# Performance work log

Measured on AMD Instinct MI355X. Metric: run time of the kernel, lower is better.

## Reference

```python
import jax, jax.numpy as jnp
import numpy as np

N_NODES = 50000
N_EDGES = 800000
IN_CH = 256
H1, D1 = 4, 64   # layer 1: 4 heads x 64 -> 256
H2, D2 = 1, 64   # output layer: 1 head x 64
NEG_SLOPE = 0.2  # DGL GATConv default


def _leaky_relu(x):
    return jnp.where(x >= 0, x, NEG_SLOPE * x)


def gat_conv(h, src, dst, W, attn_l, attn_r, bias, res_W, num_heads, out_feats, apply_elu):
    """DGL GATConv (eval mode, feat_drop=attn_drop=0).
    h: (N, F_in); src/dst: (E,) edge endpoints (edge u->v aggregates at v).
    W: (F_in, H*D); attn_l/attn_r: (H, D); bias: (H*D,); res_W: (F_in, H*D) or None.
    Returns (N, H, D).
    """
    N = h.shape[0]
    ft = (h @ W).reshape(N, num_heads, out_feats)            # (N,H,D)
    el = jnp.sum(ft * attn_l, axis=-1)                        # (N,H)
    er = jnp.sum(ft * attn_r, axis=-1)                        # (N,H)
    e = _leaky_relu(el[src] + er[dst])                        # (E,H)
    # segment softmax over incoming edges of each dst node
    emax = jax.ops.segment_max(e, dst, num_segments=N)        # (N,H)
    emax = jax.lax.stop_gradient(emax)
    ee = jnp.exp(e - emax[dst])                               # (E,H)
    denom = jax.ops.segment_sum(ee, dst, num_segments=N)      # (N,H)
    a = ee / denom[dst]                                       # (E,H)
    msg = ft[src] * a[:, :, None]                             # (E,H,D)
    rst = jax.ops.segment_sum(msg, dst, num_segments=N)       # (N,H,D)
    if res_W is not None:
        rst = rst + (h @ res_W).reshape(N, num_heads, out_feats)
    rst = rst + bias.reshape(num_heads, out_feats)
    if apply_elu:
        rst = jax.nn.elu(rst)
    return rst


def setup_inputs() -> dict:
    key = jax.random.key(0)
    ks = jax.random.split(key, 12)
    feat = jax.random.normal(ks[0], (N_NODES, IN_CH), dtype=jnp.float32)
    src = jax.random.randint(ks[1], (N_EDGES,), 0, N_NODES)
    dst = jax.random.randint(ks[2], (N_EDGES,), 0, N_NODES)
    s = 0.1
    W1 = jax.random.normal(ks[3], (IN_CH, H1 * D1), dtype=jnp.float32) * s
    al1 = jax.random.normal(ks[4], (H1, D1), dtype=jnp.float32) * s
    ar1 = jax.random.normal(ks[5], (H1, D1), dtype=jnp.float32) * s
    b1 = jnp.zeros((H1 * D1,), dtype=jnp.float32)
    W2 = jax.random.normal(ks[6], (H1 * D1, H2 * D2), dtype=jnp.float32) * s
    al2 = jax.random.normal(ks[7], (H2, D2), dtype=jnp.float32) * s
    ar2 = jax.random.normal(ks[8], (H2, D2), dtype=jnp.float32) * s
    b2 = jnp.zeros((H2 * D2,), dtype=jnp.float32)
    resW2 = jax.random.normal(ks[9], (H1 * D1, H2 * D2), dtype=jnp.float32) * s
    return {"feat": feat, "src": src, "dst": dst,
            "W1": W1, "al1": al1, "ar1": ar1, "b1": b1,
            "W2": W2, "al2": al2, "ar2": ar2, "b2": b2, "resW2": resW2}


def reference(feat, src, dst, W1, al1, ar1, b1, W2, al2, ar2, b2, resW2):
    # Layer 1: 4 heads, ELU, no residual (first DGL layer built without residual)
    h = gat_conv(feat, src, dst, W1, al1, ar1, b1, None, H1, D1, True)
    h = h.reshape(N_NODES, H1 * D1)  # flatten(1)
    # Layer 2: 1 head, residual (linear res_fc since 256 != 64), no activation
    h = gat_conv(h, src, dst, W2, al2, ar2, b2, resW2, H2, D2, False)
    return h.mean(axis=1)  # mean over output heads -> (N, out_channels)
```

## Files before the change

### kernel.cpp

```cpp
#include <hip/hip_runtime.h>
#include <math.h>

#define N_NODES 50000
#define N_EDGES 800000
#define ELL_W 64
#define CNT_STRIDE 16

#define E_SPLIT 400000
#define CONV_BLKS 1792
#define SCAT_BLKS 512

typedef __attribute__((ext_vector_type(8))) short bf16x8;
typedef __attribute__((ext_vector_type(4))) float f32x4;

__device__ __forceinline__ float leaky(float x) { return x >= 0.f ? x : 0.2f * x; }
__device__ __forceinline__ unsigned short f2bf(float f) {
  unsigned u = __float_as_uint(f);
  return (unsigned short)((u + 0x7fffu + ((u >> 16) & 1u)) >> 16);
}
__device__ __forceinline__ float bflo(unsigned u) { return __uint_as_float(u << 16); }
__device__ __forceinline__ float bfhi(unsigned u) { return __uint_as_float(u & 0xffff0000u); }
__device__ __forceinline__ unsigned pack2(float a, float b) {
  return (unsigned)f2bf(a) | ((unsigned)f2bf(b) << 16);
}

__device__ __forceinline__ void scat4(const int* __restrict__ src, const int* __restrict__ dst,
                                      int* __restrict__ cnt, unsigned short* __restrict__ ell,
                                      int e) {
  int4 d4 = *(const int4*)(dst + e);
  int4 s4 = *(const int4*)(src + e);
  int sl;
  sl = atomicAdd(cnt + d4.x * CNT_STRIDE, 1);
  if (sl < ELL_W) __builtin_nontemporal_store((unsigned short)s4.x, ell + d4.x * ELL_W + sl);
  sl = atomicAdd(cnt + d4.y * CNT_STRIDE, 1);
  if (sl < ELL_W) __builtin_nontemporal_store((unsigned short)s4.y, ell + d4.y * ELL_W + sl);
  sl = atomicAdd(cnt + d4.z * CNT_STRIDE, 1);
  if (sl < ELL_W) __builtin_nontemporal_store((unsigned short)s4.z, ell + d4.z * ELL_W + sl);
  sl = atomicAdd(cnt + d4.w * CNT_STRIDE, 1);
  if (sl < ELL_W) __builtin_nontemporal_store((unsigned short)s4.w, ell + d4.w * ELL_W + sl);
}

__launch_bounds__(256)
__global__ void prep_k(const float* __restrict__ feat, const float* __restrict__ W1,
                       const float* __restrict__ W2, const float* __restrict__ resW2,
                       short* __restrict__ featb, short* __restrict__ Wt1,
                       short* __restrict__ Wt2, const int* __restrict__ src,
                       const int* __restrict__ dst, int* __restrict__ cnt,
                       unsigned short* __restrict__ ell) {
  if (blockIdx.x < SCAT_BLKS) {
    const int gtid = blockIdx.x * 256 + threadIdx.x;
    const int gsz = SCAT_BLKS * 256;
    for (int q = gtid; q < E_SPLIT / 4; q += gsz) scat4(src, dst, cnt, ell, q * 4);
    return;
  }
  const int gtid = (blockIdx.x - SCAT_BLKS) * 256 + threadIdx.x;
  const int gsz = CONV_BLKS * 256;
  for (int idx = gtid; idx < 256 * 256; idx += gsz) {
    int n = idx >> 8, k = idx & 255;
    Wt1[idx] = (short)f2bf(W1[(size_t)k * 256 + n]);
  }
  for (int idx = gtid; idx < 128 * 256; idx += gsz) {
    int n = idx >> 8, k = idx & 255;
    float v = (n < 64) ? W2[(size_t)k * 64 + n] : resW2[(size_t)k * 64 + (n - 64)];
    Wt2[idx] = (short)f2bf(v);
  }
  const float4* f4 = (const float4*)feat;
  uint2* fb2 = (uint2*)featb;
  for (int idx = gtid; idx < N_NODES * 64; idx += gsz) {
    float4 f = f4[idx];
    uint2 o;
    o.x = pack2(f.x, f.y);
    o.y = pack2(f.z, f.w);
    fb2[idx] = o;
  }
}

template <int MODE, bool SCAT>
__launch_bounds__(256)
__global__ void mfma_gemm_k(const short* __restrict__ A, const short* __restrict__ Bt,
                            const float* __restrict__ bias, const float* __restrict__ al,
                            const float* __restrict__ ar, float* __restrict__ elp,
                            float* __restrict__ erp, short* __restrict__ Cb,
                            float* __restrict__ Cf, const int* __restrict__ src,
                            const int* __restrict__ dst, int* __restrict__ cnt,
                            unsigned short* __restrict__ ell, int M, int K, int N) {
  constexpr int EPI_COLS = (MODE == 0) ? 136 : 72;
  union SharedU {
    struct { short As[4][128][8]; short Bs[4][128][8]; } ab;
    short epi[128 * EPI_COLS];
  };
  __shared__ SharedU sh;

  if (SCAT && blockIdx.y == 0) {
    const int gtid = blockIdx.x * 256 + threadIdx.x;
    const int gsz = gridDim.x * 256;
    for (int q = gtid; q < (N_EDGES - E_SPLIT) / 4; q += gsz)
      scat4(src, dst, cnt, ell, E_SPLIT + q * 4);
    return;
  }
  const int tid = threadIdx.x;
  const int bm0 = blockIdx.x * 128;
  const int bn0 = (SCAT ? ((int)blockIdx.y - 1) : (int)blockIdx.y) * 128;
  const int wave = tid >> 6, lane = tid & 63;
  const int wm = (wave & 1) * 64, wn = (wave >> 1) * 64;
  const int q = lane >> 4, r16 = lane & 15;
  const int srow = tid >> 1, sk = (tid & 1) * 16, sq = (tid & 1) * 2;
  f32x4 acc[4][4] = {};

  for (int k0 = 0; k0 < K; k0 += 32) {
    {
      uint4 v0 = {0, 0, 0, 0}, v1 = {0, 0, 0, 0};
      if (bm0 + srow < M) {
        const uint4* p = (const uint4*)(A + (size_t)(bm0 + srow) * K + k0 + sk);
        v0 = p[0];
        v1 = p[1];
      }
      *(uint4*)&sh.ab.As[sq][srow][0] = v0;
      *(uint4*)&sh.ab.As[sq + 1][srow][0] = v1;
    }
    {
      const uint4* p = (const uint4*)(Bt + (size_t)(bn0 + srow) * K + k0 + sk);
      *(uint4*)&sh.ab.Bs[sq][srow][0] = p[0];
      *(uint4*)&sh.ab.Bs[sq + 1][srow][0] = p[1];
    }
    __syncthreads();
    bf16x8 af[4], bfr[4];
#pragma unroll
    for (int i = 0; i < 4; ++i) af[i] = *(const bf16x8*)&sh.ab.As[q][wm + i * 16 + r16][0];
#pragma unroll
    for (int j = 0; j < 4; ++j) bfr[j] = *(const bf16x8*)&sh.ab.Bs[q][wn + j * 16 + r16][0];
#pragma unroll
    for (int i = 0; i < 4; ++i)
#pragma unroll
      for (int j = 0; j < 4; ++j)
        acc[i][j] = __builtin_amdgcn_mfma_f32_16x16x32_bf16(af[i], bfr[j], acc[i][j], 0, 0, 0);
    __syncthreads();
  }

  if (MODE == 0 || wn == 0) {
    const int head = (bn0 + wn) >> 6;
    float alv[4], arv[4];
#pragma unroll
    for (int j = 0; j < 4; ++j) {
      alv[j] = al[((MODE == 0) ? head * 64 : 0) + j * 16 + r16];
      arv[j] = ar[((MODE == 0) ? head * 64 : 0) + j * 16 + r16];
    }
#pragma unroll
    for (int i = 0; i < 4; ++i) {
#pragma unroll
      for (int reg = 0; reg < 4; ++reg) {
        float dl = acc[i][0][reg] * alv[0] + acc[i][1][reg] * alv[1] +
                   acc[i][2][reg] * alv[2] + acc[i][3][reg] * alv[3];
        float dr = acc[i][0][reg] * arv[0] + acc[i][1][reg] * arv[1] +
                   acc[i][2][reg] * arv[2] + acc[i][3][reg] * arv[3];
#pragma unroll
        for (int mm = 1; mm < 16; mm <<= 1) {
          dl += __shfl_xor(dl, mm);
          dr += __shfl_xor(dr, mm);
        }
        int row_g = bm0 + wm + i * 16 + q * 4 + reg;
        if (r16 == 0 && row_g < M) {
          if (MODE == 0) {
            elp[(size_t)row_g * 4 + head] = dl;
            erp[(size_t)row_g * 4 + head] = dr;
          } else {
            elp[row_g] = dl;
            erp[row_g] = dr;
          }
        }
      }
    }
  }

  if (MODE == 0) {
#pragma unroll
    for (int i = 0; i < 4; ++i)
#pragma unroll
      for (int reg = 0; reg < 4; ++reg) {
        int row = wm + i * 16 + q * 4 + reg;
#pragma unroll
        for (int j = 0; j < 4; ++j)
          sh.epi[row * EPI_COLS + wn + j * 16 + r16] = (short)f2bf(acc[i][j][reg]);
      }
    __syncthreads();
#pragma unroll
    for (int k = 0; k < 8; ++k) {
      int c = k * 256 + tid;
      int row = c >> 4, cc = c & 15;
      int row_g = bm0 + row;
      if (row_g < M) {
        uint4 v = *(const uint4*)&sh.epi[row * EPI_COLS + cc * 8];
        *(uint4*)(Cb + (size_t)row_g * N + bn0 + cc * 8) = v;
      }
    }
  } else {
    if (wn == 0) {
#pragma unroll
      for (int i = 0; i < 4; ++i)
#pragma unroll
        for (int reg = 0; reg < 4; ++reg) {
          int row = wm + i * 16 + q * 4 + reg;
#pragma unroll
          for (int j = 0; j < 4; ++j)
            sh.epi[row * EPI_COLS + j * 16 + r16] = (short)f2bf(acc[i][j][reg]);
        }
    } else {
#pragma unroll
      for (int i = 0; i < 4; ++i)
#pragma unroll
        for (int reg = 0; reg < 4; ++reg) {
          int row_g = bm0 + wm + i * 16 + q * 4 + reg;
          if (row_g >= M) continue;
#pragma unroll
          for (int j = 0; j < 4; ++j) {
            int col = j * 16 + r16;
            Cf[(size_t)row_g * 64 + col] = acc[i][j][reg] + bias[col];
          }
        }
    }
    __syncthreads();
#pragma unroll
    for (int k = 0; k < 4; ++k) {
      int c = k * 256 + tid;
      int row = c >> 3, cc = c & 7;
      int row_g = bm0 + row;
      if (row_g < M) {
        uint4 v = *(const uint4*)&sh.epi[row * EPI_COLS + cc * 8];
        *(uint4*)(Cb + (size_t)row_g * 64 + cc * 8) = v;
      }
    }
  }
}

__launch_bounds__(256)
__global__ void agg1_k(const unsigned short* __restrict__ ell, const int* __restrict__ cnt,
                       const float* __restrict__ el, const float* __restrict__ er,
                       const short* __restrict__ ft, const float* __restrict__ bias,
                       short* __restrict__ h1) {
  int node = blockIdx.x * 4 + (threadIdx.x >> 6);
  int lane = threadIdx.x & 63;
  if (node >= N_NODES) return;
  int deg = min(cnt[node * CNT_STRIDE], ELL_W);
  const unsigned short* row = ell + node * ELL_W;
  const int half = lane >> 5, l5 = lane & 31, h = l5 >> 3;
  float erh = er[(size_t)node * 4 + h];
  float denom = 0.f;
  float acc[8] = {0.f, 0.f, 0.f, 0.f, 0.f, 0.f, 0.f, 0.f};
  int i = 0;
  for (; i + 8 <= deg; i += 8) {
    int s[4];
#pragma unroll
    for (int k = 0; k < 4; ++k) s[k] = row[i + k * 2 + half];
    float e[4];
#pragma unroll
    for (int k = 0; k < 4; ++k) e[k] = leaky(el[(size_t)s[k] * 4 + h] + erh);
    uint4 u[4];
#pragma unroll
    for (int k = 0; k < 4; ++k) u[k] = *(const uint4*)(ft + (size_t)s[k] * 256 + l5 * 8);
    float w[4];
#pragma unroll
    for (int k = 0; k < 4; ++k) w[k] = __expf(e[k]);
#pragma unroll
    for (int k = 0; k < 4; ++k) {
      denom += w[k];
      acc[0] += w[k] * bflo(u[k].x);
      acc[1] += w[k] * bfhi(u[k].x);
      acc[2] += w[k] * bflo(u[k].y);
      acc[3] += w[k] * bfhi(u[k].y);
      acc[4] += w[k] * bflo(u[k].z);
      acc[5] += w[k] * bfhi(u[k].z);
      acc[6] += w[k] * bflo(u[k].w);
      acc[7] += w[k] * bfhi(u[k].w);
    }
  }
  for (; i < deg; i += 2) {
    int idx = i + half;
    bool v = idx < deg;
    int s = v ? (int)row[idx] : (int)row[i];
    float e = leaky(el[(size_t)s * 4 + h] + erh);
    uint4 u = *(const uint4*)(ft + (size_t)s * 256 + l5 * 8);
    float w = v ? __expf(e) : 0.f;
    denom += w;
    acc[0] += w * bflo(u.x);
    acc[1] += w * bfhi(u.x);
    acc[2] += w * bflo(u.y);
    acc[3] += w * bfhi(u.y);
    acc[4] += w * bflo(u.z);
    acc[5] += w * bfhi(u.z);
    acc[6] += w * bflo(u.w);
    acc[7] += w * bfhi(u.w);
  }
  denom += __shfl_xor(denom, 32);
#pragma unroll
  for (int k = 0; k < 8; ++k) acc[k] += __shfl_xor(acc[k], 32);
  if (half == 0) {
    float inv = (deg > 0) ? 1.f / denom : 0.f;
    float4 b0 = *(const float4*)(bias + l5 * 8);
    float4 b1 = *(const float4*)(bias + l5 * 8 + 4);
    float v[8];
    v[0] = acc[0] * inv + b0.x;
    v[1] = acc[1] * inv + b0.y;
    v[2] = acc[2] * inv + b0.z;
    v[3] = acc[3] * inv + b0.w;
    v[4] = acc[4] * inv + b1.x;
    v[5] = acc[5] * inv + b1.y;
    v[6] = acc[6] * inv + b1.z;
    v[7] = acc[7] * inv + b1.w;
#pragma unroll
    for (int k = 0; k < 8; ++k) v[k] = v[k] > 0.f ? v[k] : expm1f(v[k]);
    uint4 o;
    o.x = pack2(v[0], v[1]);
    o.y = pack2(v[2], v[3]);
    o.z = pack2(v[4], v[5]);
    o.w = pack2(v[6], v[7]);
    *(uint4*)(h1 + (size_t)node * 256 + l5 * 8) = o;
  }
}

__launch_bounds__(256)
__global__ void agg2_k(const unsigned short* __restrict__ ell, const int* __restrict__ cnt,
                       const float* __restrict__ el, const float* __restrict__ er,
                       const short* __restrict__ ft, float* __restrict__ out) {
  int node = blockIdx.x * 4 + (threadIdx.x >> 6);
  int lane = threadIdx.x & 63;
  if (node >= N_NODES) return;
  int deg = min(cnt[node * CNT_STRIDE], ELL_W);
  const unsigned short* row = ell + node * ELL_W;
  const int qtr = lane >> 4, l4 = lane & 15;
  float erd = er[node];
  float denom = 0.f;
  float acc[4] = {0.f, 0.f, 0.f, 0.f};
  int i = 0;
  for (; i + 8 <= deg; i += 8) {
    int s0 = row[i + qtr], s1 = row[i + 4 + qtr];
    float e0 = leaky(el[s0] + erd), e1 = leaky(el[s1] + erd);
    uint2 u0 = *(const uint2*)(ft + (size_t)s0 * 64 + l4 * 4);
    uint2 u1 = *(const uint2*)(ft + (size_t)s1 * 64 + l4 * 4);
    float w0 = __expf(e0), w1 = __expf(e1);
    denom += w0 + w1;
    acc[0] += w0 * bflo(u0.x) + w1 * bflo(u1.x);
    acc[1] += w0 * bfhi(u0.x) + w1 * bfhi(u1.x);
    acc[2] += w0 * bflo(u0.y) + w1 * bflo(u1.y);
    acc[3] += w0 * bfhi(u0.y) + w1 * bfhi(u1.y);
  }
  for (; i < deg; i += 4) {
    int idx = i + qtr;
    bool v = idx < deg;
    int s = v ? (int)row[idx] : (int)row[i];
    float e = leaky(el[s] + erd);
    uint2 u = *(const uint2*)(ft + (size_t)s * 64 + l4 * 4);
    float w = v ? __expf(e) : 0.f;
    denom += w;
    acc[0] += w * bflo(u.x);
    acc[1] += w * bfhi(u.x);
    acc[2] += w * bflo(u.y);
    acc[3] += w * bfhi(u.y);
  }
  denom += __shfl_xor(denom, 16);
  denom += __shfl_xor(denom, 32);
#pragma unroll
  for (int k = 0; k < 4; ++k) {
    acc[k] += __shfl_xor(acc[k], 16);
    acc[k] += __shfl_xor(acc[k], 32);
  }
  if (lane < 16) {
    float inv = (deg > 0) ? 1.f / denom : 0.f;
    float4* po = (float4*)(out + (size_t)node * 64 + l4 * 4);
    float4 o = *po;
    o.x += acc[0] * inv;
    o.y += acc[1] * inv;
    o.z += acc[2] * inv;
    o.w += acc[3] * inv;
    *po = o;
  }
}

extern "C" void kernel_launch(void* const* d_in, const int* in_sizes, int n_in,
                              void* d_out, int out_size, void* d_ws, size_t ws_size,
                              hipStream_t stream) {
  const float* feat  = (const float*)d_in[0];
  const int*   src   = (const int*)d_in[1];
  const int*   dst   = (const int*)d_in[2];
  const float* W1    = (const float*)d_in[3];
  const float* al1   = (const float*)d_in[4];
  const float* ar1   = (const float*)d_in[5];
  const float* b1    = (const float*)d_in[6];
  const float* W2    = (const float*)d_in[7];
  const float* al2   = (const float*)d_in[8];
  const float* ar2   = (const float*)d_in[9];
  const float* b2    = (const float*)d_in[10];
  const float* resW2 = (const float*)d_in[11];
  float* out = (float*)d_out;

  char* p = (char*)d_ws;
  short* featb = (short*)p; p += (size_t)N_NODES * 256 * 2;
  short* ft1b = (short*)p; p += (size_t)N_NODES * 256 * 2;
  short* h1b  = (short*)p; p += (size_t)N_NODES * 256 * 2;
  short* ft2b = (short*)p; p += (size_t)N_NODES * 64 * 2;
  short* Wt1  = (short*)p; p += 256 * 256 * 2;
  short* Wt2  = (short*)p; p += 128 * 256 * 2;
  float* el1  = (float*)p; p += (size_t)N_NODES * 4 * 4;
  float* er1  = (float*)p; p += (size_t)N_NODES * 4 * 4;
  float* el2  = (float*)p; p += (size_t)N_NODES * 4;
  float* er2  = (float*)p; p += (size_t)N_NODES * 4;
  int* cnt    = (int*)p;   p += (size_t)N_NODES * CNT_STRIDE * 4;
  unsigned short* ell = (unsigned short*)p; p += (size_t)N_NODES * ELL_W * 2;

  hipMemsetAsync(cnt, 0, (size_t)N_NODES * CNT_STRIDE * sizeof(int), stream);

  dim3 blk(256);

  prep_k<<<SCAT_BLKS + CONV_BLKS, blk, 0, stream>>>(feat, W1, W2, resW2, featb, Wt1, Wt2,
                                                    src, dst, cnt, ell);

  mfma_gemm_k<0, true><<<dim3(391, 3), blk, 0, stream>>>(
      featb, Wt1, nullptr, al1, ar1, el1, er1, ft1b, nullptr,
      src, dst, cnt, ell, N_NODES, 256, 256);
  agg1_k<<<12500, blk, 0, stream>>>(ell, cnt, el1, er1, ft1b, b1, h1b);

  mfma_gemm_k<1, false><<<dim3(391, 1), blk, 0, stream>>>(
      h1b, Wt2, b2, al2, ar2, el2, er2, ft2b, out,
      nullptr, nullptr, nullptr, nullptr, N_NODES, 256, 128);
  agg2_k<<<12500, blk, 0, stream>>>(ell, cnt, el2, er2, ft2b, out);
}
```

Baseline: 279.0 us.

## Precompute normalized attention weights per node in LDS before feature gather

```diff
diff --git a/kernel.cpp b/kernel.cpp
--- a/kernel.cpp
+++ b/kernel.cpp
@@ -12,6 +12,7 @@
 
 typedef __attribute__((ext_vector_type(8))) short bf16x8;
 typedef __attribute__((ext_vector_type(4))) float f32x4;
+typedef __attribute__((ext_vector_type(2))) float f32x2;
 
 __device__ __forceinline__ float leaky(float x) { return x >= 0.f ? x : 0.2f * x; }
 __device__ __forceinline__ unsigned short f2bf(float f) {
@@ -237,75 +238,93 @@
                        const float* __restrict__ el, const float* __restrict__ er,
                        const short* __restrict__ ft, const float* __restrict__ bias,
                        short* __restrict__ h1) {
-  int node = blockIdx.x * 4 + (threadIdx.x >> 6);
-  int lane = threadIdx.x & 63;
+  __shared__ unsigned wofs[4][64];
+  __shared__ float wval[4][4][64];
+  const int nib = threadIdx.x >> 6;
+  const int node = blockIdx.x * 4 + nib;
+  const int lane = threadIdx.x & 63;
   if (node >= N_NODES) return;
-  int deg = min(cnt[node * CNT_STRIDE], ELL_W);
+  const int deg = min(cnt[node * CNT_STRIDE], ELL_W);
   const unsigned short* row = ell + node * ELL_W;
+
+  {
+    int s_raw = row[lane];
+    bool val = lane < deg;
+    int s0 = deg > 0 ? (int)row[0] : 0;
+    int s_safe = val ? s_raw : s0;
+    float4 el4 = *(const float4*)(el + (size_t)s_safe * 4);
+    float4 er4 = *(const float4*)(er + (size_t)node * 4);
+    float w0 = val ? __expf(leaky(el4.x + er4.x)) : 0.f;
+    float w1 = val ? __expf(leaky(el4.y + er4.y)) : 0.f;
+    float w2 = val ? __expf(leaky(el4.z + er4.z)) : 0.f;
+    float w3 = val ? __expf(leaky(el4.w + er4.w)) : 0.f;
+    float d0 = w0, d1 = w1, d2 = w2, d3 = w3;
+#pragma unroll
+    for (int m = 1; m < 64; m <<= 1) {
+      d0 += __shfl_xor(d0, m);
+      d1 += __shfl_xor(d1, m);
+      d2 += __shfl_xor(d2, m);
+      d3 += __shfl_xor(d3, m);
+    }
+    float i0 = deg > 0 ? 1.f / d0 : 0.f;
+    float i1 = deg > 0 ? 1.f / d1 : 0.f;
+    float i2 = deg > 0 ? 1.f / d2 : 0.f;
+    float i3 = deg > 0 ? 1.f / d3 : 0.f;
+    wofs[nib][lane] = (unsigned)s_safe * 512u;
+    wval[nib][0][lane] = w0 * i0;
+    wval[nib][1][lane] = w1 * i1;
+    wval[nib][2][lane] = w2 * i2;
+    wval[nib][3][lane] = w3 * i3;
+  }
+
   const int half = lane >> 5, l5 = lane & 31, h = l5 >> 3;
-  float erh = er[(size_t)node * 4 + h];
-  float denom = 0.f;
-  float acc[8] = {0.f, 0.f, 0.f, 0.f, 0.f, 0.f, 0.f, 0.f};
-  int i = 0;
-  for (; i + 8 <= deg; i += 8) {
-    int s[4];
-#pragma unroll
-    for (int k = 0; k < 4; ++k) s[k] = row[i + k * 2 + half];
-    float e[4];
-#pragma unroll
-    for (int k = 0; k < 4; ++k) e[k] = leaky(el[(size_t)s[k] * 4 + h] + erh);
+  const char* ftb = (const char*)ft + l5 * 16;
+  const float* wv = &wval[nib][h][0];
+  const unsigned* wo = &wofs[nib][0];
+  f32x2 acc2[4] = {};
+  const int degR = (deg + 7) & ~7;
+  for (int i = 0; i < degR; i += 8) {
+    unsigned o[4];
+    float w[4];
     uint4 u[4];
 #pragma unroll
-    for (int k = 0; k < 4; ++k) u[k] = *(const uint4*)(ft + (size_t)s[k] * 256 + l5 * 8);
-    float w[4];
-#pragma unroll
-    for (int k = 0; k < 4; ++k) w[k] = __expf(e[k]);
-#pragma unroll
     for (int k = 0; k < 4; ++k) {
-      denom += w[k];
-      acc[0] += w[k] * bflo(u[k].x);
-      acc[1] += w[k] * bfhi(u[k].x);
-      acc[2] += w[k] * bflo(u[k].y);
-      acc[3] += w[k] * bfhi(u[k].y);
-      acc[4] += w[k] * bflo(u[k].z);
-      acc[5] += w[k] * bfhi(u[k].z);
-      acc[6] += w[k] * bflo(u[k].w);
-      acc[7] += w[k] * bfhi(u[k].w);
-    }
-  }
-  for (; i < deg; i += 2) {
-    int idx = i + half;
-    bool v = idx < deg;
-    int s = v ? (int)row[idx] : (int)row[i];
-    float e = leaky(el[(size_t)s * 4 + h] + erh);
-    uint4 u = *(const uint4*)(ft + (size_t)s * 256 + l5 * 8);
-    float w = v ? __expf(e) : 0.f;
-    denom += w;
-    acc[0] += w * bflo(u.x);
-    acc[1] += w * bfhi(u.x);
-    acc[2] += w * bflo(u.y);
-    acc[3] += w * bfhi(u.y);
-    acc[4] += w * bflo(u.z);
-    acc[5] += w * bfhi(u.z);
-    acc[6] += w * bflo(u.w);
-    acc[7] += w * bfhi(u.w);
-  }
-  denom += __shfl_xor(denom, 32);
-#pragma unroll
-  for (int k = 0; k < 8; ++k) acc[k] += __shfl_xor(acc[k], 32);
+      int slot = i + k * 2 + half;
+      o[k] = wo[slot];
+      w[k] = wv[slot];
+    }
+#pragma unroll
+    for (int k = 0; k < 4; ++k) u[k] = *(const uint4*)(ftb + o[k]);
+#pragma unroll
+    for (int k = 0; k < 4; ++k) {
+      f32x2 w2 = {w[k], w[k]};
+      f32x2 p0 = {bflo(u[k].x), bfhi(u[k].x)};
+      f32x2 p1 = {bflo(u[k].y), bfhi(u[k].y)};
+      f32x2 p2 = {bflo(u[k].z), bfhi(u[k].z)};
+      f32x2 p3 = {bflo(u[k].w), bfhi(u[k].w)};
+      acc2[0] += w2 * p0;
+      acc2[1] += w2 * p1;
+      acc2[2] += w2 * p2;
+      acc2[3] += w2 * p3;
+    }
+  }
+#pragma unroll
+  for (int j = 0; j < 4; ++j) {
+    acc2[j][0] += __shfl_xor(acc2[j][0], 32);
+    acc2[j][1] += __shfl_xor(acc2[j][1], 32);
+  }
   if (half == 0) {
-    float inv = (deg > 0) ? 1.f / denom : 0.f;
     float4 b0 = *(const float4*)(bias + l5 * 8);
     float4 b1 = *(const float4*)(bias + l5 * 8 + 4);
     float v[8];
-    v[0] = acc[0] * inv + b0.x;
-    v[1] = acc[1] * inv + b0.y;
-    v[2] = acc[2] * inv + b0.z;
-    v[3] = acc[3] * inv + b0.w;
-    v[4] = acc[4] * inv + b1.x;
-    v[5] = acc[5] * inv + b1.y;
-    v[6] = acc[6] * inv + b1.z;
-    v[7] = acc[7] * inv + b1.w;
+    v[0] = acc2[0][0] + b0.x;
+    v[1] = acc2[0][1] + b0.y;
+    v[2] = acc2[1][0] + b0.z;
+    v[3] = acc2[1][1] + b0.w;
+    v[4] = acc2[2][0] + b1.x;
+    v[5] = acc2[2][1] + b1.y;
+    v[6] = acc2[3][0] + b1.z;
+    v[7] = acc2[3][1] + b1.w;
 #pragma unroll
     for (int k = 0; k < 8; ++k) v[k] = v[k] > 0.f ? v[k] : expm1f(v[k]);
     uint4 o;
@@ -321,56 +340,64 @@
 __global__ void agg2_k(const unsigned short* __restrict__ ell, const int* __restrict__ cnt,
                        const float* __restrict__ el, const float* __restrict__ er,
                        const short* __restrict__ ft, float* __restrict__ out) {
-  int node = blockIdx.x * 4 + (threadIdx.x >> 6);
-  int lane = threadIdx.x & 63;
+  __shared__ uint2 wsl[4][64];
+  const int nib = threadIdx.x >> 6;
+  const int node = blockIdx.x * 4 + nib;
+  const int lane = threadIdx.x & 63;
   if (node >= N_NODES) return;
-  int deg = min(cnt[node * CNT_STRIDE], ELL_W);
+  const int deg = min(cnt[node * CNT_STRIDE], ELL_W);
   const unsigned short* row = ell + node * ELL_W;
+
+  {
+    int s_raw = row[lane];
+    bool val = lane < deg;
+    int s0 = deg > 0 ? (int)row[0] : 0;
+    int s_safe = val ? s_raw : s0;
+    float erd = er[node];
+    float w = val ? __expf(leaky(el[s_safe] + erd)) : 0.f;
+    float d = w;
+#pragma unroll
+    for (int m = 1; m < 64; m <<= 1) d += __shfl_xor(d, m);
+    float inv = deg > 0 ? 1.f / d : 0.f;
+    uint2 e;
+    e.x = (unsigned)s_safe * 128u;
+    e.y = __float_as_uint(w * inv);
+    wsl[nib][lane] = e;
+  }
+
   const int qtr = lane >> 4, l4 = lane & 15;
-  float erd = er[node];
-  float denom = 0.f;
-  float acc[4] = {0.f, 0.f, 0.f, 0.f};
-  int i = 0;
-  for (; i + 8 <= deg; i += 8) {
-    int s0 = row[i + qtr], s1 = row[i + 4 + qtr];
-    float e0 = leaky(el[s0] + erd), e1 = leaky(el[s1] + erd);
-    uint2 u0 = *(const uint2*)(ft + (size_t)s0 * 64 + l4 * 4);
-    uint2 u1 = *(const uint2*)(ft + (size_t)s1 * 64 + l4 * 4);
-    float w0 = __expf(e0), w1 = __expf(e1);
-    denom += w0 + w1;
-    acc[0] += w0 * bflo(u0.x) + w1 * bflo(u1.x);
-    acc[1] += w0 * bfhi(u0.x) + w1 * bfhi(u1.x);
-    acc[2] += w0 * bflo(u0.y) + w1 * bflo(u1.y);
-    acc[3] += w0 * bfhi(u0.y) + w1 * bfhi(u1.y);
-  }
-  for (; i < deg; i += 4) {
-    int idx = i + qtr;
-    bool v = idx < deg;
-    int s = v ? (int)row[idx] : (int)row[i];
-    float e = leaky(el[s] + erd);
-    uint2 u = *(const uint2*)(ft + (size_t)s * 64 + l4 * 4);
-    float w = v ? __expf(e) : 0.f;
-    denom += w;
-    acc[0] += w * bflo(u.x);
-    acc[1] += w * bfhi(u.x);
-    acc[2] += w * bflo(u.y);
-    acc[3] += w * bfhi(u.y);
-  }
-  denom += __shfl_xor(denom, 16);
-  denom += __shfl_xor(denom, 32);
-#pragma unroll
-  for (int k = 0; k < 4; ++k) {
-    acc[k] += __shfl_xor(acc[k], 16);
-    acc[k] += __shfl_xor(acc[k], 32);
+  const char* ftb = (const char*)ft + l4 * 8;
+  f32x2 acc2[2] = {};
+  const int degR = (deg + 7) & ~7;
+  for (int i = 0; i < degR; i += 8) {
+#pragma unroll
+    for (int k = 0; k < 2; ++k) {
+      int slot = i + k * 4 + qtr;
+      uint2 e = wsl[nib][slot];
+      uint2 u = *(const uint2*)(ftb + e.x);
+      float w = __uint_as_float(e.y);
+      f32x2 w2 = {w, w};
+      f32x2 p0 = {bflo(u.x), bfhi(u.x)};
+      f32x2 p1 = {bflo(u.y), bfhi(u.y)};
+      acc2[0] += w2 * p0;
+      acc2[1] += w2 * p1;
+    }
+  }
+#pragma unroll
+  for (int j = 0; j < 2; ++j) {
+#pragma unroll
+    for (int c = 0; c < 2; ++c) {
+      acc2[j][c] += __shfl_xor(acc2[j][c], 16);
+      acc2[j][c] += __shfl_xor(acc2[j][c], 32);
+    }
   }
   if (lane < 16) {
-    float inv = (deg > 0) ? 1.f / denom : 0.f;
     float4* po = (float4*)(out + (size_t)node * 64 + l4 * 4);
     float4 o = *po;
-    o.x += acc[0] * inv;
-    o.y += acc[1] * inv;
-    o.z += acc[2] * inv;
-    o.w += acc[3] * inv;
+    o.x += acc2[0][0];
+    o.y += acc2[0][1];
+    o.z += acc2[1][0];
+    o.w += acc2[1][1];
     *po = o;
   }
 }
```

New measurement: 275.7 us. Within noise of the previous version (-1.2%).
